# Kernel tuning notes

Measured on AMD Instinct MI355X. Metric: run time of the kernel, lower is better.

## Reference

```python
import jax, jax.numpy as jnp
import numpy as np

DIM = 768
HEADS = 12
HEAD_DIM = DIM // HEADS
EPS_ATTN = 1e-6
LN_EPS = 1e-5


def _piece_weight():
    # BlockDistanceConv with num_patches_per_side=16, patch_group_size=16 -> 4x4 blocks
    bps = 4
    centers = np.array([[i + 0.5, j + 0.5] for i in range(bps) for j in range(bps)], dtype=np.float32)
    d = np.linalg.norm(centers[:, None, :] - centers[None, :, :], axis=-1)
    mat = np.cos(d / d.max() * np.pi / 4.0)  # 'cos' transform
    mat = mat / mat.sum(axis=0, keepdims=True)
    return jnp.asarray(mat, dtype=jnp.float32)  # [16, 16], out = W @ x over piece channels


def setup_inputs() -> dict:
    key = jax.random.key(0)
    ks = jax.random.split(key, 4)
    B, N, W, C = 128, 16, 16, DIM
    x = jax.random.normal(ks[0], (B, N, W, C), dtype=jnp.float32)
    ln_gamma = jnp.ones((C,), dtype=jnp.float32)
    ln_beta = jnp.zeros((C,), dtype=jnp.float32)
    w_qkv = jax.random.normal(ks[1], (C, 3 * C), dtype=jnp.float32) * (C ** -0.5)
    w_out = jax.random.normal(ks[2], (C, C), dtype=jnp.float32) * (C ** -0.5)
    b_out = jnp.zeros((C,), dtype=jnp.float32)
    w_piece = _piece_weight()
    return {"x": x, "ln_gamma": ln_gamma, "ln_beta": ln_beta, "w_qkv": w_qkv,
            "w_out": w_out, "b_out": b_out, "w_piece": w_piece}


def reference(x, ln_gamma, ln_beta, w_qkv, w_out, b_out, w_piece):
    B, N, W, C = x.shape
    H, D = HEADS, HEAD_DIM
    # LayerNorm over channel dim
    mu = jnp.mean(x, axis=-1, keepdims=True)
    var = jnp.mean((x - mu) ** 2, axis=-1, keepdims=True)
    xn = (x - mu) * jax.lax.rsqrt(var + LN_EPS) * ln_gamma + ln_beta
    # qkv projection (no bias)
    qkv = xn @ w_qkv  # [B,N,W,3C]
    q, k, v = jnp.split(qkv, 3, axis=-1)
    # relu kernel feature map
    q = jax.nn.relu(q) + EPS_ATTN
    k = jax.nn.relu(k) + EPS_ATTN
    # split heads: 'b n w (h d) -> b h n w d'
    def heads(t):
        return t.reshape(B, N, W, H, D).transpose(0, 3, 1, 2, 4)
    q, k, v = heads(q), heads(k), heads(v)
    # per-window kv = k^T v  (sum over window positions w)  -> [B,H,N,D,D]
    kv = jnp.einsum('bhnwd,bhnwe->bhnde', k, v)
    # BlockDistanceConv: 1x1 conv mixing over piece dim N with fixed weights
    kv = jnp.einsum('ij,bhjde->bhide', w_piece, kv)
    # out = q @ kv  -> [B,H,N,W,D]
    out = jnp.einsum('bhnwd,bhnde->bhnwe', q, kv)
    # merge heads: 'b h n w d -> b n w (h d)'
    out = out.transpose(0, 2, 3, 1, 4).reshape(B, N, W, H * D)
    # output projection (dropout is identity in eval)
    return out @ w_out + b_out
```

## Files before the change

### kernel.cpp

```cpp
#include <hip/hip_runtime.h>

#define DIM 768
#define HEADS 12
#define TOK 32768

typedef unsigned short ushort_t;
typedef __attribute__((ext_vector_type(8))) short short8v;
typedef __attribute__((ext_vector_type(4))) float f32x4;
typedef __attribute__((ext_vector_type(4))) unsigned short us4;

__device__ __forceinline__ ushort_t f2bf(float x) {
  union { float f; unsigned u; } c; c.f = x;
  unsigned r = (c.u + 0x7FFFu + ((c.u >> 16) & 1u)) >> 16;
  return (ushort_t)r;
}

__device__ __forceinline__ void gload_lds16(const void* g, void* l) {
  __builtin_amdgcn_global_load_lds((const __attribute__((address_space(1))) void*)g,
                                   (__attribute__((address_space(3))) void*)l, 16, 0, 0);
}

#define FENCE asm volatile("" ::: "memory")
#define BARRIER do { FENCE; __builtin_amdgcn_s_barrier(); FENCE; } while (0)
#define LGK0 asm volatile("s_waitcnt lgkmcnt(0)" ::: "memory")

__global__ __launch_bounds__(256) void ln_kernel(const float* __restrict__ x,
                                                 const float* __restrict__ g,
                                                 const float* __restrict__ be,
                                                 ushort_t* __restrict__ xn) {
  int t = blockIdx.x;
  int tid = threadIdx.x;
  const float* row = x + (size_t)t * DIM;
  float v0 = row[tid], v1 = row[tid + 256], v2 = row[tid + 512];
  float s  = v0 + v1 + v2;
  float sq = v0 * v0 + v1 * v1 + v2 * v2;
  #pragma unroll
  for (int off = 32; off; off >>= 1) {
    s  += __shfl_down(s, off);
    sq += __shfl_down(sq, off);
  }
  __shared__ float ls[4], lq[4];
  int wid = tid >> 6, lane = tid & 63;
  if (lane == 0) { ls[wid] = s; lq[wid] = sq; }
  __syncthreads();
  s  = ls[0] + ls[1] + ls[2] + ls[3];
  sq = lq[0] + lq[1] + lq[2] + lq[3];
  float mu  = s * (1.0f / DIM);
  float var = sq * (1.0f / DIM) - mu * mu;
  float rs  = rsqrtf(var + 1e-5f);
  ushort_t* orow = xn + (size_t)t * DIM;
  orow[tid]       = f2bf((v0 - mu) * rs * g[tid]       + be[tid]);
  orow[tid + 256] = f2bf((v1 - mu) * rs * g[tid + 256] + be[tid + 256]);
  orow[tid + 512] = f2bf((v2 - mu) * rs * g[tid + 512] + be[tid + 512]);
}

__global__ __launch_bounds__(256) void convT(const float* __restrict__ src,
                                             ushort_t* __restrict__ dst, int R, int Ccol) {
  __shared__ float tile[32][33];
  int c0 = blockIdx.x * 32, r0 = blockIdx.y * 32;
  int tx = threadIdx.x & 31, ty = threadIdx.x >> 5;
  #pragma unroll
  for (int i = 0; i < 32; i += 8)
    tile[ty + i][tx] = src[(size_t)(r0 + ty + i) * Ccol + c0 + tx];
  __syncthreads();
  #pragma unroll
  for (int i = 0; i < 32; i += 8)
    dst[(size_t)(c0 + ty + i) * R + r0 + tx] = f2bf(tile[tx][ty + i]);
}

__global__ __launch_bounds__(512, 2) void gemm_8ph(const ushort_t* __restrict__ A,
                                                   const ushort_t* __restrict__ Bt,
                                                   ushort_t* __restrict__ qbf,
                                                   ushort_t* __restrict__ kbf,
                                                   ushort_t* __restrict__ vTbf) {
  extern __shared__ __align__(16) char lds[];
  const int Kb = DIM * 2;
  const int N = 3 * DIM;
  const int nbn = N / 256;
  const size_t GHalf = (size_t)64 * Kb;

  int bid = blockIdx.x;
  int qd = gridDim.x >> 3;
  int wid = (bid & 7) * qd + (bid >> 3);
  int bm = wid / nbn, bn = wid % nbn;
  int row0 = bm * 256, col0 = bn * 256;
  int t = threadIdx.x;
  int lane = t & 63, wave = t >> 6;
  int wr = wave >> 2, wc = wave & 3;

  const char* Ag = (const char*)A + (size_t)row0 * Kb;
  const char* Bg = (const char*)Bt + (size_t)col0 * Kb;

  int o0 = t * 16;
  int sr = o0 >> 7;
  int skb = (o0 & 127) ^ ((sr & 7) << 4);
  size_t goff = (size_t)sr * Kb + skb;

  #define STG(Gbase, Lbase, kt)                                               \
    do {                                                                      \
      gload_lds16((Gbase) + goff + (size_t)(kt) * 128, lds + (Lbase) + o0);   \
      gload_lds16((Gbase) + goff + GHalf + (size_t)(kt) * 128,                \
                  lds + (Lbase) + o0 + 8192);                                 \
    } while (0)

  int fr = lane & 15, fkb = (lane >> 4) << 4;
  int swz = (fr & 7) << 4;
  int kb0 = fkb ^ swz;
  int kb1 = (64 + fkb) ^ swz;
  int laA = (wr * 128 + fr) * 128;
  int laB = 32768 + (wc * 64 + fr) * 128;

  #define LOAD_A(dst, dbase, mq)                                              \
    _Pragma("unroll") for (int mi = 0; mi < 4; ++mi) {                        \
      dst[mi][0] = *(const short8v*)(lds + (dbase) + laA + (mq)*8192 + mi*2048 + kb0); \
      dst[mi][1] = *(const short8v*)(lds + (dbase) + laA + (mq)*8192 + mi*2048 + kb1); \
    }
  #define LOAD_B(dst, dbase, nq)                                              \
    _Pragma("unroll") for (int ni = 0; ni < 2; ++ni) {                        \
      dst[ni][0] = *(const short8v*)(lds + (dbase) + laB + (nq)*4096 + ni*2048 + kb0); \
      dst[ni][1] = *(const short8v*)(lds + (dbase) + laB + (nq)*4096 + ni*2048 + kb1); \
    }
  #define MFMA16(av, bv, mq, nq)                                              \
    do {                                                                      \
      __builtin_amdgcn_s_setprio(1);                                          \
      _Pragma("unroll") for (int mi = 0; mi < 4; ++mi)                        \
        _Pragma("unroll") for (int ni = 0; ni < 2; ++ni) {                    \
          acc[(mq)*4+mi][(nq)*2+ni] = __builtin_amdgcn_mfma_f32_16x16x32_bf16(\
              av[mi][0], bv[ni][0], acc[(mq)*4+mi][(nq)*2+ni], 0, 0, 0);      \
          acc[(mq)*4+mi][(nq)*2+ni] = __builtin_amdgcn_mfma_f32_16x16x32_bf16(\
              av[mi][1], bv[ni][1], acc[(mq)*4+mi][(nq)*2+ni], 0, 0, 0);      \
        }                                                                     \
      __builtin_amdgcn_s_setprio(0);                                          \
    } while (0)

  STG(Ag, 0, 0);  STG(Ag + 128 * Kb, 16384, 0);
  STG(Bg, 32768, 0);  STG(Bg + 128 * Kb, 49152, 0);
  STG(Ag, 65536, 1);  STG(Ag + 128 * Kb, 65536 + 16384, 1);
  STG(Bg, 65536 + 32768, 1);
  asm volatile("s_waitcnt vmcnt(6)" ::: "memory");
  __builtin_amdgcn_s_barrier();

  f32x4 acc[8][4] = {};
  for (int it = 0; it < 6; ++it) {
    const int d0 = 0, d1 = 65536;
    int t1k = 2 * it + 1, t2k = 2 * it + 2, t3k = 2 * it + 3;
    bool st = (it < 5);
    short8v ar[4][2], a2[4][2], br[2][2], b2[2][2];
    LOAD_A(ar, d0, 0); LOAD_B(br, d0, 0);
    STG(Bg + 128 * Kb, d1 + 49152, t1k);
    BARRIER; LGK0; MFMA16(ar, br, 0, 0); BARRIER;
    LOAD_A(a2, d0, 1);
    BARRIER; LGK0; MFMA16(a2, br, 1, 0); BARRIER;
    LOAD_B(b2, d0, 1);
    if (st) { STG(Ag, d0, t2k); STG(Ag + 128 * Kb, d0 + 16384, t2k); }
    BARRIER; LGK0; MFMA16(ar, b2, 0, 1); BARRIER;
    if (st) STG(Bg, d0 + 32768, t2k);
    BARRIER; LGK0; MFMA16(a2, b2, 1, 1);
    if (st) asm volatile("s_waitcnt vmcnt(6)" ::: "memory");
    else    asm volatile("s_waitcnt vmcnt(0)" ::: "memory");
    BARRIER;
    LOAD_A(ar, d1, 0); LOAD_B(br, d1, 0);
    if (st) STG(Bg + 128 * Kb, d0 + 49152, t2k);
    BARRIER; LGK0; MFMA16(ar, br, 0, 0); BARRIER;
    LOAD_A(a2, d1, 1);
    BARRIER; LGK0; MFMA16(a2, br, 1, 0); BARRIER;
    LOAD_B(b2, d1, 1);
    if (st) { STG(Ag, d1, t3k); STG(Ag + 128 * Kb, d1 + 16384, t3k); }
    BARRIER; LGK0; MFMA16(ar, b2, 0, 1); BARRIER;
    if (st) STG(Bg, d1 + 32768, t3k);
    BARRIER; LGK0; MFMA16(a2, b2, 1, 1);
    if (st) asm volatile("s_waitcnt vmcnt(6)" ::: "memory");
    BARRIER;
  }
  #undef STG
  #undef LOAD_A
  #undef LOAD_B
  #undef MFMA16

  int rbase = row0 + wr * 128 + ((lane >> 4) << 2);
  int cbase = col0 + wc * 64 + fr;
  #pragma unroll
  for (int m = 0; m < 8; ++m) {
    int r0r = rbase + m * 16;
    #pragma unroll
    for (int n = 0; n < 4; ++n) {
      int c = cbase + n * 16;
      if (c < DIM) {
        #pragma unroll
        for (int j = 0; j < 4; ++j)
          qbf[(size_t)(r0r + j) * DIM + c] = f2bf(fmaxf(acc[m][n][j], 0.0f) + 1e-6f);
      } else if (c < 2 * DIM) {
        #pragma unroll
        for (int j = 0; j < 4; ++j)
          kbf[(size_t)(r0r + j) * DIM + (c - DIM)] = f2bf(fmaxf(acc[m][n][j], 0.0f) + 1e-6f);
      } else {
        int ch = c - 2 * DIM;
        int hh = ch >> 6, e = ch & 63;
        int bb = r0r >> 8, rr = r0r & 255;
        us4 pk;
        #pragma unroll
        for (int j = 0; j < 4; ++j) pk[j] = f2bf(acc[m][n][j]);
        *(us4*)&vTbf[((((size_t)bb * HEADS + hh) * 64 + e) << 8) + rr] = pk;
      }
    }
  }
}

__global__ __launch_bounds__(512, 2) void gemm_out8(const ushort_t* __restrict__ A,
                                                    const ushort_t* __restrict__ Bt,
                                                    const float* __restrict__ bias,
                                                    float* __restrict__ C) {
  extern __shared__ __align__(16) char lds[];
  const int Kb = DIM * 2;
  const int N = DIM;
  const int nbn = N / 128;
  const size_t GHalf = (size_t)64 * Kb;

  int bid = blockIdx.x;
  int qd = gridDim.x >> 3;
  int wid = (bid & 7) * qd + (bid >> 3);
  int bm = wid / nbn, bn = wid % nbn;
  int row0 = bm * 256, col0 = bn * 128;
  int t = threadIdx.x;
  int lane = t & 63, wave = t >> 6;
  int wr = wave >> 2, wc = wave & 3;

  const char* Ag = (const char*)A + (size_t)row0 * Kb;
  const char* Bg = (const char*)Bt + (size_t)col0 * Kb;

  int o0 = t * 16;
  int sr = o0 >> 7;
  int skb = (o0 & 127) ^ ((sr & 7) << 4);
  size_t goff = (size_t)sr * Kb + skb;

  #define STGA(Gbase, Lbase, kt)                                              \
    do {                                                                      \
      gload_lds16((Gbase) + goff + (size_t)(kt) * 128, lds + (Lbase) + o0);   \
      gload_lds16((Gbase) + goff + GHalf + (size_t)(kt) * 128,                \
                  lds + (Lbase) + o0 + 8192);                                 \
    } while (0)
  #define STGB(Gbase, Lbase, kt)                                              \
    gload_lds16((Gbase) + goff + (size_t)(kt) * 128, lds + (Lbase) + o0)

  int fr = lane & 15, fkb = (lane >> 4) << 4;
  int swz = (fr & 7) << 4;
  int kb0 = fkb ^ swz;
  int kb1 = (64 + fkb) ^ swz;
  int laA = (wr * 128 + fr) * 128;
  int laB = 32768 + (wc * 32 + fr) * 128;

  #define LOAD_A(dst, dbase, mq)                                              \
    _Pragma("unroll") for (int mi = 0; mi < 4; ++mi) {                        \
      dst[mi][0] = *(const short8v*)(lds + (dbase) + laA + (mq)*8192 + mi*2048 + kb0); \
      dst[mi][1] = *(const short8v*)(lds + (dbase) + laA + (mq)*8192 + mi*2048 + kb1); \
    }
  #define LOAD_B(dst, dbase, nq)                                              \
    do {                                                                      \
      dst[0] = *(const short8v*)(lds + (dbase) + laB + (nq)*2048 + kb0);      \
      dst[1] = *(const short8v*)(lds + (dbase) + laB + (nq)*2048 + kb1);      \
    } while (0)
  #define MFMA8(av, bv, mq, nq)                                               \
    do {                                                                      \
      __builtin_amdgcn_s_setprio(1);                                          \
      _Pragma("unroll") for (int mi = 0; mi < 4; ++mi) {                      \
        acc[(mq)*4+mi][nq] = __builtin_amdgcn_mfma_f32_16x16x32_bf16(         \
            av[mi][0], bv[0], acc[(mq)*4+mi][nq], 0, 0, 0);                   \
        acc[(mq)*4+mi][nq] = __builtin_amdgcn_mfma_f32_16x16x32_bf16(         \
            av[mi][1], bv[1], acc[(mq)*4+mi][nq], 0, 0, 0);                   \
      }                                                                       \
      __builtin_amdgcn_s_setprio(0);                                          \
    } while (0)

  STGA(Ag, 0, 0);  STGA(Ag + 128 * Kb, 16384, 0);
  STGB(Bg, 32768, 0);  STGB(Bg + GHalf, 32768 + 8192, 0);
  STGA(Ag, 49152, 1);  STGA(Ag + 128 * Kb, 49152 + 16384, 1);
  STGB(Bg, 49152 + 32768, 1);
  asm volatile("s_waitcnt vmcnt(5)" ::: "memory");
  __builtin_amdgcn_s_barrier();

  f32x4 acc[8][2] = {};
  for (int it = 0; it < 6; ++it) {
    const int d0 = 0, d1 = 49152;
    int t1k = 2 * it + 1, t2k = 2 * it + 2, t3k = 2 * it + 3;
    bool st = (it < 5);
    short8v ar[4][2], a2[4][2], br[2], b2[2];
    LOAD_A(ar, d0, 0); LOAD_B(br, d0, 0);
    STGB(Bg + GHalf, d1 + 32768 + 8192, t1k);
    BARRIER; LGK0; MFMA8(ar, br, 0, 0); BARRIER;
    LOAD_A(a2, d0, 1);
    BARRIER; LGK0; MFMA8(a2, br, 1, 0); BARRIER;
    LOAD_B(b2, d0, 1);
    if (st) { STGA(Ag, d0, t2k); STGA(Ag + 128 * Kb, d0 + 16384, t2k); }
    BARRIER; LGK0; MFMA8(ar, b2, 0, 1); BARRIER;
    if (st) STGB(Bg, d0 + 32768, t2k);
    BARRIER; LGK0; MFMA8(a2, b2, 1, 1);
    if (st) asm volatile("s_waitcnt vmcnt(5)" ::: "memory");
    else    asm volatile("s_waitcnt vmcnt(0)" ::: "memory");
    BARRIER;
    LOAD_A(ar, d1, 0); LOAD_B(br, d1, 0);
    if (st) STGB(Bg + GHalf, d0 + 32768 + 8192, t2k);
    BARRIER; LGK0; MFMA8(ar, br, 0, 0); BARRIER;
    LOAD_A(a2, d1, 1);
    BARRIER; LGK0; MFMA8(a2, br, 1, 0); BARRIER;
    LOAD_B(b2, d1, 1);
    if (st) { STGA(Ag, d1, t3k); STGA(Ag + 128 * Kb, d1 + 16384, t3k); }
    BARRIER; LGK0; MFMA8(ar, b2, 0, 1); BARRIER;
    if (st) STGB(Bg, d1 + 32768, t3k);
    BARRIER; LGK0; MFMA8(a2, b2, 1, 1);
    if (st) asm volatile("s_waitcnt vmcnt(5)" ::: "memory");
    BARRIER;
  }
  #undef STGA
  #undef STGB
  #undef LOAD_A
  #undef LOAD_B
  #undef MFMA8

  int rbase = row0 + wr * 128 + ((lane >> 4) << 2);
  int cbase = col0 + wc * 32 + fr;
  #pragma unroll
  for (int m = 0; m < 8; ++m) {
    #pragma unroll
    for (int n = 0; n < 2; ++n) {
      int c = cbase + n * 16;
      float bz = bias[c];
      #pragma unroll
      for (int j = 0; j < 4; ++j)
        C[(size_t)(rbase + m * 16 + j) * N + c] = acc[m][n][j] + bz;
    }
  }
}

__global__ __launch_bounds__(512) void attn_fused(const ushort_t* __restrict__ qbf,
                                                  const ushort_t* __restrict__ kbf,
                                                  const ushort_t* __restrict__ vTbf,
                                                  const float* __restrict__ wp,
                                                  ushort_t* __restrict__ attnO) {
  extern __shared__ __align__(16) char lds[];
  const int QOFF = 65536, SOFF = 73728;
  int bh = blockIdx.x;
  int b = bh / HEADS, h = bh % HEADS;
  int t = threadIdx.x;
  int lane = t & 63, wave = t >> 6;
  int fr = lane & 15, fkb = (lane >> 4) << 4;
  int lg4 = (lane >> 4) << 2;

  const char* qg = (const char*)(qbf + ((size_t)b * 256) * DIM + h * 64);
  const char* kg = (const char*)(kbf + ((size_t)b * 256) * DIM + h * 64);
  const char* vg = (const char*)(vTbf + ((size_t)bh << 14));

  #pragma unroll
  for (int is = 0; is < 4; ++is) {
    int o = is * 8192 + t * 16;
    int r = o >> 7;
    int byt = (o & 127) ^ ((r & 7) << 4);
    gload_lds16(kg + (size_t)r * (DIM * 2) + byt, lds + o);
  }
  #pragma unroll
  for (int is = 0; is < 4; ++is) {
    int o = is * 8192 + t * 16;
    int e = o >> 9;
    int byt = (o & 511) ^ ((e & 7) << 4);
    gload_lds16(vg + e * 512 + byt, lds + 32768 + o);
  }
  {
    int o = t * 16;
    int r = o >> 7;
    int byt = (o & 127) ^ ((r & 7) << 4);
    gload_lds16(qg + (size_t)r * (DIM * 2) + byt, lds + QOFF + o);
  }
  asm volatile("s_waitcnt vmcnt(0)" ::: "memory");
  __builtin_amdgcn_s_barrier();

  int wrs = wave & 3, wcs = wave >> 2;
  int wrp = wave >> 2, wcp = wave & 3;

  for (int q4 = 0; q4 < 4; ++q4) {
    f32x4 accA[4][2] = {};
    {
      short8v kf[4][2], qf[2][2];
      #pragma unroll
      for (int mi = 0; mi < 4; ++mi)
        #pragma unroll
        for (int ks = 0; ks < 2; ++ks) {
          int r = wrs * 64 + mi * 16 + fr;
          kf[mi][ks] = *(const short8v*)(lds + r * 128 + ((ks * 64 + fkb) ^ ((r & 7) << 4)));
        }
      #pragma unroll
      for (int ni = 0; ni < 2; ++ni)
        #pragma unroll
        for (int ks = 0; ks < 2; ++ks) {
          int r = wcs * 32 + ni * 16 + fr;
          qf[ni][ks] = *(const short8v*)(lds + QOFF + r * 128 + ((ks * 64 + fkb) ^ ((r & 7) << 4)));
        }
      #pragma unroll
      for (int mi = 0; mi < 4; ++mi)
        #pragma unroll
        for (int ni = 0; ni < 2; ++ni)
          #pragma unroll
          for (int ks = 0; ks < 2; ++ks)
            accA[mi][ni] = __builtin_amdgcn_mfma_f32_16x16x32_bf16(kf[mi][ks], qf[ni][ks],
                                                                   accA[mi][ni], 0, 0, 0);
    }
    BARRIER;
    #pragma unroll
    for (int mi = 0; mi < 4; ++mi)
      #pragma unroll
      for (int ni = 0; ni < 2; ++ni) {
        float wpf = wp[(q4 * 4 + wcs * 2 + ni) * 16 + wrs * 4 + mi];
        us4 pk;
        #pragma unroll
        for (int j = 0; j < 4; ++j) pk[j] = f2bf(accA[mi][ni][j] * wpf);
        int qrow = wcs * 32 + ni * 16 + fr;
        int sbyte = (wrs * 64 + mi * 16 + lg4) * 2;
        *(us4*)(lds + SOFF + qrow * 512 + (sbyte ^ ((qrow & 7) << 4))) = pk;
      }
    if (q4 < 3) {
      int o = t * 16;
      int r = o >> 7;
      int byt = (o & 127) ^ ((r & 7) << 4);
      gload_lds16(qg + (size_t)((q4 + 1) * 64 + r) * (DIM * 2) + byt, lds + QOFF + o);
    }
    LGK0;
    BARRIER;
    f32x4 accB[2] = {{0.f,0.f,0.f,0.f},{0.f,0.f,0.f,0.f}};
    #pragma unroll
    for (int ks = 0; ks < 8; ++ks) {
      int kb = ks * 64 + fkb;
      int e = wcp * 16 + fr;
      short8v bv = *(const short8v*)(lds + 32768 + e * 512 + (kb ^ ((e & 7) << 4)));
      #pragma unroll
      for (int mt = 0; mt < 2; ++mt) {
        int r = wrp * 32 + mt * 16 + fr;
        short8v av = *(const short8v*)(lds + SOFF + r * 512 + (kb ^ ((r & 7) << 4)));
        accB[mt] = __builtin_amdgcn_mfma_f32_16x16x32_bf16(av, bv, accB[mt], 0, 0, 0);
      }
    }
    #pragma unroll
    for (int mt = 0; mt < 2; ++mt) {
      int row = b * 256 + q4 * 64 + wrp * 32 + mt * 16 + lg4;
      int col = h * 64 + wcp * 16 + fr;
      #pragma unroll
      for (int j = 0; j < 4; ++j)
        attnO[(size_t)(row + j) * DIM + col] = f2bf(accB[mt][j]);
    }
    if (q4 < 3) asm volatile("s_waitcnt vmcnt(8)" ::: "memory");
    BARRIER;
  }
}

extern "C" void kernel_launch(void* const* d_in, const int* in_sizes, int n_in,
                              void* d_out, int out_size, void* d_ws, size_t ws_size,
                              hipStream_t stream) {
  const float* x    = (const float*)d_in[0];
  const float* g    = (const float*)d_in[1];
  const float* be   = (const float*)d_in[2];
  const float* wqkv = (const float*)d_in[3];
  const float* wout = (const float*)d_in[4];
  const float* bout = (const float*)d_in[5];
  const float* wp   = (const float*)d_in[6];
  float* out = (float*)d_out;

  char* w = (char*)d_ws;
  const size_t SZ = (size_t)TOK * DIM * 2;
  ushort_t* qbf   = (ushort_t*)(w);
  ushort_t* kbf   = (ushort_t*)(w + SZ);
  ushort_t* vTbf  = (ushort_t*)(w + 2 * SZ);
  ushort_t* xn    = (ushort_t*)(w + 3 * SZ);
  ushort_t* wqkvT = (ushort_t*)(w + 4 * SZ);
  ushort_t* woutT = (ushort_t*)(w + 4 * SZ + 3538944);
  ushort_t* attnO = xn;

  (void)hipFuncSetAttribute(reinterpret_cast<const void*>(&gemm_8ph),
                            hipFuncAttributeMaxDynamicSharedMemorySize, 131072);
  (void)hipFuncSetAttribute(reinterpret_cast<const void*>(&gemm_out8),
                            hipFuncAttributeMaxDynamicSharedMemorySize, 98304);
  (void)hipFuncSetAttribute(reinterpret_cast<const void*>(&attn_fused),
                            hipFuncAttributeMaxDynamicSharedMemorySize, 106496);

  dim3 gt1(3 * DIM / 32, DIM / 32);
  convT<<<gt1, 256, 0, stream>>>(wqkv, wqkvT, DIM, 3 * DIM);
  dim3 gt2(DIM / 32, DIM / 32);
  convT<<<gt2, 256, 0, stream>>>(wout, woutT, DIM, DIM);

  ln_kernel<<<TOK, 256, 0, stream>>>(x, g, be, xn);

  gemm_8ph<<<(TOK / 256) * (3 * DIM / 256), 512, 131072, stream>>>(
      xn, wqkvT, qbf, kbf, vTbf);

  attn_fused<<<128 * HEADS, 512, 106496, stream>>>(qbf, kbf, vTbf, wp, attnO);

  gemm_out8<<<(TOK / 256) * (DIM / 128), 512, 98304, stream>>>(
      attnO, woutT, bout, out);
}
```

Before: 301.7 us.

## Software-pipeline LDS fragment loads against MFMA in both GEMM main loops

New measurement: 306.0 us. About the same (+1.4%).

```diff
diff --git a/kernel.cpp b/kernel.cpp
--- a/kernel.cpp
+++ b/kernel.cpp
@@ -139,37 +139,48 @@
   STG(Bg, 65536 + 32768, 1);
   asm volatile("s_waitcnt vmcnt(6)" ::: "memory");
   __builtin_amdgcn_s_barrier();
+  FENCE;
+
+  short8v aR0[4][2], aR1[4][2], bR0[2][2], bR1[2][2];
+  LOAD_A(aR0, 0, 0); LOAD_B(bR0, 0, 0);
 
   f32x4 acc[8][4] = {};
   for (int it = 0; it < 6; ++it) {
     const int d0 = 0, d1 = 65536;
     int t1k = 2 * it + 1, t2k = 2 * it + 2, t3k = 2 * it + 3;
     bool st = (it < 5);
-    short8v ar[4][2], a2[4][2], br[2][2], b2[2][2];
-    LOAD_A(ar, d0, 0); LOAD_B(br, d0, 0);
+    LOAD_A(aR1, d0, 1);
     STG(Bg + 128 * Kb, d1 + 49152, t1k);
-    BARRIER; LGK0; MFMA16(ar, br, 0, 0); BARRIER;
-    LOAD_A(a2, d0, 1);
-    BARRIER; LGK0; MFMA16(a2, br, 1, 0); BARRIER;
-    LOAD_B(b2, d0, 1);
+    MFMA16(aR0, bR0, 0, 0);
+    BARRIER;
+    LOAD_B(bR1, d0, 1);
+    MFMA16(aR1, bR0, 1, 0);
+    BARRIER;
     if (st) { STG(Ag, d0, t2k); STG(Ag + 128 * Kb, d0 + 16384, t2k); }
-    BARRIER; LGK0; MFMA16(ar, b2, 0, 1); BARRIER;
+    MFMA16(aR0, bR1, 0, 1);
+    if (st) asm volatile("s_waitcnt vmcnt(4)" ::: "memory");
+    else    asm volatile("s_waitcnt vmcnt(0)" ::: "memory");
+    BARRIER;
+    LOAD_A(aR0, d1, 0); LOAD_B(bR0, d1, 0);
     if (st) STG(Bg, d0 + 32768, t2k);
-    BARRIER; LGK0; MFMA16(a2, b2, 1, 1);
-    if (st) asm volatile("s_waitcnt vmcnt(6)" ::: "memory");
-    else    asm volatile("s_waitcnt vmcnt(0)" ::: "memory");
-    BARRIER;
-    LOAD_A(ar, d1, 0); LOAD_B(br, d1, 0);
+    MFMA16(aR1, bR1, 1, 1);
+    BARRIER;
+    LOAD_A(aR1, d1, 1);
     if (st) STG(Bg + 128 * Kb, d0 + 49152, t2k);
-    BARRIER; LGK0; MFMA16(ar, br, 0, 0); BARRIER;
-    LOAD_A(a2, d1, 1);
-    BARRIER; LGK0; MFMA16(a2, br, 1, 0); BARRIER;
-    LOAD_B(b2, d1, 1);
+    MFMA16(aR0, bR0, 0, 0);
+    BARRIER;
+    LOAD_B(bR1, d1, 1);
+    MFMA16(aR1, bR0, 1, 0);
+    BARRIER;
     if (st) { STG(Ag, d1, t3k); STG(Ag + 128 * Kb, d1 + 16384, t3k); }
-    BARRIER; LGK0; MFMA16(ar, b2, 0, 1); BARRIER;
-    if (st) STG(Bg, d1 + 32768, t3k);
-    BARRIER; LGK0; MFMA16(a2, b2, 1, 1);
-    if (st) asm volatile("s_waitcnt vmcnt(6)" ::: "memory");
+    MFMA16(aR0, bR1, 0, 1);
+    if (st) asm volatile("s_waitcnt vmcnt(4)" ::: "memory");
+    BARRIER;
+    if (st) {
+      LOAD_A(aR0, d0, 0); LOAD_B(bR0, d0, 0);
+      STG(Bg, d1 + 32768, t3k);
+    }
+    MFMA16(aR1, bR1, 1, 1);
     BARRIER;
   }
   #undef STG
@@ -277,37 +288,48 @@
   STGB(Bg, 49152 + 32768, 1);
   asm volatile("s_waitcnt vmcnt(5)" ::: "memory");
   __builtin_amdgcn_s_barrier();
+  FENCE;
+
+  short8v aR0[4][2], aR1[4][2], bR0[2], bR1[2];
+  LOAD_A(aR0, 0, 0); LOAD_B(bR0, 0, 0);
 
   f32x4 acc[8][2] = {};
   for (int it = 0; it < 6; ++it) {
     const int d0 = 0, d1 = 49152;
     int t1k = 2 * it + 1, t2k = 2 * it + 2, t3k = 2 * it + 3;
     bool st = (it < 5);
-    short8v ar[4][2], a2[4][2], br[2], b2[2];
-    LOAD_A(ar, d0, 0); LOAD_B(br, d0, 0);
+    LOAD_A(aR1, d0, 1);
     STGB(Bg + GHalf, d1 + 32768 + 8192, t1k);
-    BARRIER; LGK0; MFMA8(ar, br, 0, 0); BARRIER;
-    LOAD_A(a2, d0, 1);
-    BARRIER; LGK0; MFMA8(a2, br, 1, 0); BARRIER;
-    LOAD_B(b2, d0, 1);
+    MFMA8(aR0, bR0, 0, 0);
+    BARRIER;
+    LOAD_B(bR1, d0, 1);
+    MFMA8(aR1, bR0, 1, 0);
+    BARRIER;
     if (st) { STGA(Ag, d0, t2k); STGA(Ag + 128 * Kb, d0 + 16384, t2k); }
-    BARRIER; LGK0; MFMA8(ar, b2, 0, 1); BARRIER;
+    MFMA8(aR0, bR1, 0, 1);
+    if (st) asm volatile("s_waitcnt vmcnt(4)" ::: "memory");
+    else    asm volatile("s_waitcnt vmcnt(0)" ::: "memory");
+    BARRIER;
+    LOAD_A(aR0, d1, 0); LOAD_B(bR0, d1, 0);
     if (st) STGB(Bg, d0 + 32768, t2k);
-    BARRIER; LGK0; MFMA8(a2, b2, 1, 1);
-    if (st) asm volatile("s_waitcnt vmcnt(5)" ::: "memory");
-    else    asm volatile("s_waitcnt vmcnt(0)" ::: "memory");
-    BARRIER;
-    LOAD_A(ar, d1, 0); LOAD_B(br, d1, 0);
+    MFMA8(aR1, bR1, 1, 1);
+    BARRIER;
+    LOAD_A(aR1, d1, 1);
     if (st) STGB(Bg + GHalf, d0 + 32768 + 8192, t2k);
-    BARRIER; LGK0; MFMA8(ar, br, 0, 0); BARRIER;
-    LOAD_A(a2, d1, 1);
-    BARRIER; LGK0; MFMA8(a2, br, 1, 0); BARRIER;
-    LOAD_B(b2, d1, 1);
+    MFMA8(aR0, bR0, 0, 0);
+    BARRIER;
+    LOAD_B(bR1, d1, 1);
+    MFMA8(aR1, bR0, 1, 0);
+    BARRIER;
     if (st) { STGA(Ag, d1, t3k); STGA(Ag + 128 * Kb, d1 + 16384, t3k); }
-    BARRIER; LGK0; MFMA8(ar, b2, 0, 1); BARRIER;
-    if (st) STGB(Bg, d1 + 32768, t3k);
-    BARRIER; LGK0; MFMA8(a2, b2, 1, 1);
-    if (st) asm volatile("s_waitcnt vmcnt(5)" ::: "memory");
+    MFMA8(aR0, bR1, 0, 1);
+    if (st) asm volatile("s_waitcnt vmcnt(4)" ::: "memory");
+    BARRIER;
+    if (st) {
+      LOAD_A(aR0, d0, 0); LOAD_B(bR0, d0, 0);
+      STGB(Bg, d1 + 32768, t3k);
+    }
+    MFMA8(aR1, bR1, 1, 1);
     BARRIER;
   }
   #undef STGA
```
